# Performance work log

Measured on AMD Instinct MI355X. Metric: run time of the kernel, lower is better.

The kernel has to match this reference:

```python
import jax, jax.numpy as jnp
import numpy as np

B, W, IN, H, Z, D = 32, 256, 4096, 1024, 100, 100


def setup_inputs() -> dict:
    key = jax.random.key(0)
    ks = jax.random.split(key, 10)
    s = lambda k, shape, sc=0.02: jax.random.normal(k, shape, dtype=jnp.float32) * sc
    return {
        "x": jax.random.normal(ks[0], (B, W, IN), jnp.float32),
        # GRU params (torch layout: gates ordered r, z, n)
        "W_ih": s(ks[1], (3 * H, IN)),
        "W_hh": s(ks[2], (3 * H, H)),
        "b_ih": jnp.zeros((3 * H,), jnp.float32),
        "b_hh": jnp.zeros((3 * H,), jnp.float32),
        # dense / mu / sigma heads
        "Wd": s(ks[3], (D, Z + H)),
        "bd": jnp.zeros((D,), jnp.float32),
        "Wmu": s(ks[4], (Z, D)),
        "bmu": jnp.zeros((Z,), jnp.float32),
        "Wsig": s(ks[5], (Z, D)),
        "bsig": jnp.zeros((Z,), jnp.float32),
        # planar normalizing flow
        "u": jax.random.normal(ks[6], (1,), jnp.float32),
        "Wpnf": s(ks[7], (Z, Z)),
        "bpnf": jnp.zeros((Z,), jnp.float32),
        # torch.rand_like -> uniform [0,1), one draw per timestep: [W, B, Z]
        "noise": jax.random.uniform(ks[8], (W, B, Z), jnp.float32),
    }


def reference(x, W_ih, W_hh, b_ih, b_hh, Wd, bd, Wmu, bmu, Wsig, bsig, u, Wpnf, bpnf, noise):
    Bv = x.shape[0]
    Hd = W_hh.shape[1]
    Zd = Wmu.shape[0]
    # hoist input projection out of the recurrence: [W, B, 3H]
    xW = jnp.einsum('bwf,gf->wbg', x, W_ih) + b_ih

    def step(carry, inp):
        h, z_t = carry
        gi, eps = inp
        gh = h @ W_hh.T + b_hh
        gi_r, gi_z, gi_n = jnp.split(gi, 3, axis=-1)
        gh_r, gh_z, gh_n = jnp.split(gh, 3, axis=-1)
        r = jax.nn.sigmoid(gi_r + gh_r)
        zg = jax.nn.sigmoid(gi_z + gh_z)
        n = jnp.tanh(gi_n + r * gh_n)
        h_new = (1.0 - zg) * n + zg * h
        dense_out = jnp.concatenate([z_t, h_new], axis=-1) @ Wd.T + bd
        mu_t = dense_out @ Wmu.T + bmu
        lv_t = jax.nn.softplus(dense_out @ Wsig.T + bsig)  # module calls this "logvar"
        z_new = mu_t + jnp.exp(0.5 * lv_t) * eps  # reparam with uniform noise (as in source)
        z_new = z_new + u * jnp.tanh(z_new @ Wpnf.T + bpnf)  # planar flow
        return (h_new, z_new), (z_new, mu_t, lv_t)

    h0 = jnp.zeros((Bv, Hd), x.dtype)
    z0 = jnp.zeros((Bv, Zd), x.dtype)
    _, (z, mu, lv) = jax.lax.scan(step, (h0, z0), (xW, noise))
    # [W,B,Z] -> [B,W,Z]
    return (jnp.swapaxes(z, 0, 1), jnp.swapaxes(mu, 0, 1), jnp.swapaxes(lv, 0, 1))
```

## Files before the change

### kernel.cpp

```cpp
#include <hip/hip_runtime.h>
#include <stdint.h>


#define MFMA16 __builtin_amdgcn_mfma_f32_16x16x32_bf16

using f32x4  = __attribute__((ext_vector_type(4))) float;
using bf16x8 = __attribute__((ext_vector_type(8))) short;

static constexpr int NB_MM  = 64;
static constexpr int NB_ALL = 65;
static constexpr int TPB    = 1024;
static constexpr int WSTEPS = 256;

static constexpr int HS_STRIDE = 1032;
static constexpr int SM_HS    = 66048;
static constexpr int SM_TOTAL = 123648;

__device__ __align__(256) unsigned short g_gi[8192u * 3072u];
__device__ __align__(256) unsigned short g_hb[2 * 32 * 1024];
__device__ __align__(256) unsigned       g_bar[64];
__device__ unsigned g_flag;

__device__ __forceinline__ float bf2f(unsigned short v){
  unsigned u = ((unsigned)v) << 16;
  return __builtin_bit_cast(float, u);
}
__device__ __forceinline__ unsigned short f2bf(float f){
  unsigned u = __builtin_bit_cast(unsigned, f);
  u += 0x7FFFu + ((u >> 16) & 1u);
  return (unsigned short)(u >> 16);
}
__device__ __forceinline__ float ldin(const void* p, size_t i){
  return g_flag ? ((const float*)p)[i] : bf2f(((const unsigned short*)p)[i]);
}
__device__ __forceinline__ unsigned short ldbf(const void* p, size_t i){
  return g_flag ? f2bf(((const float*)p)[i]) : ((const unsigned short*)p)[i];
}
__device__ __forceinline__ void stout(void* p, size_t i, float v){
  if (g_flag) ((float*)p)[i] = v;
  else        ((unsigned short*)p)[i] = f2bf(v);
}
__device__ __forceinline__ void ld16(const void* p, size_t idx,
                                     uint4* lo, uint4* hi){
  if (g_flag){
    const float* f = (const float*)p + idx;
    float4 a = *(const float4*)(f);
    float4 b = *(const float4*)(f + 4);
    float4 c = *(const float4*)(f + 8);
    float4 d = *(const float4*)(f + 12);
    unsigned short s[16];
    s[0]=f2bf(a.x); s[1]=f2bf(a.y); s[2]=f2bf(a.z); s[3]=f2bf(a.w);
    s[4]=f2bf(b.x); s[5]=f2bf(b.y); s[6]=f2bf(b.z); s[7]=f2bf(b.w);
    s[8]=f2bf(c.x); s[9]=f2bf(c.y); s[10]=f2bf(c.z); s[11]=f2bf(c.w);
    s[12]=f2bf(d.x); s[13]=f2bf(d.y); s[14]=f2bf(d.z); s[15]=f2bf(d.w);
    *lo = *(uint4*)s; *hi = *(uint4*)(s + 8);
  } else {
    const unsigned short* q = (const unsigned short*)p + idx;
    *lo = *(const uint4*)q; *hi = *(const uint4*)(q + 8);
  }
}
__device__ __forceinline__ float sigm(float x){ return 1.f / (1.f + __expf(-x)); }
__device__ __forceinline__ float sane(float x, float lim){
  return fminf(fmaxf(x, -lim), lim);
}

__global__ void k_probe(const void* noise){
  if (threadIdx.x == 0 && blockIdx.x == 0){
    const unsigned* w = (const unsigned*)noise;
    unsigned f = 0;
    for (int k = 0; k < 16; ++k)
      if ((w[k] & 0xFFFFu) > 0x3F80u) f = 1u;
    g_flag = f;
  }
}

__global__ void k_state_init(){
  int i = blockIdx.x * blockDim.x + threadIdx.x;
  if (i < 32768) ((unsigned*)g_hb)[i] = 0u;
  else if (i < 32832) g_bar[i - 32768] = 0u;
}

__global__ __launch_bounds__(256) void k_gemm_gi(
    const void* __restrict__ x,
    const void* __restrict__ Wih,
    const void* __restrict__ bih)
{
  __shared__ unsigned short As[128 * 40];
  __shared__ unsigned short Bs[128 * 40];
  const int tm = blockIdx.x & 63;
  const int tn = blockIdx.x >> 6;
  const int m0 = tm * 128, n0 = tn * 128;
  const int t  = threadIdx.x;
  const int wave = t >> 6, lane = t & 63;
  const int wm = wave & 1, wn = wave >> 1;
  const int ln = lane & 15, kg = lane >> 4;

  const int srow = t >> 1;
  const int skc  = (t & 1) * 16;
  const int m  = m0 + srow;
  const int bb = m & 31, ww = m >> 5;
  const size_t aoff = ((size_t)(bb * 256 + ww)) * 4096 + skc;
  const size_t boff = ((size_t)(n0 + srow)) * 4096 + skc;
  unsigned short* asl = &As[srow * 40 + skc];
  unsigned short* bsl = &Bs[srow * 40 + skc];

  f32x4 acc[4][4];
#pragma unroll
  for (int i = 0; i < 4; ++i)
#pragma unroll
    for (int j = 0; j < 4; ++j) acc[i][j] = (f32x4){0.f, 0.f, 0.f, 0.f};

  uint4 av, av2, bv, bv2;
  ld16(x,   aoff, &av, &av2);
  ld16(Wih, boff, &bv, &bv2);

  for (int k0 = 0; k0 < 4096; k0 += 32){
    __syncthreads();
    *(uint4*)asl = av;  *(uint4*)(asl + 8) = av2;
    *(uint4*)bsl = bv;  *(uint4*)(bsl + 8) = bv2;
    __syncthreads();
    if (k0 + 32 < 4096){
      ld16(x,   aoff + k0 + 32, &av, &av2);
      ld16(Wih, boff + k0 + 32, &bv, &bv2);
    }
    bf16x8 af[4], bfv[4];
#pragma unroll
    for (int mt = 0; mt < 4; ++mt)
      af[mt] = *(const bf16x8*)&As[(wm * 64 + mt * 16 + ln) * 40 + kg * 8];
#pragma unroll
    for (int nt = 0; nt < 4; ++nt)
      bfv[nt] = *(const bf16x8*)&Bs[(wn * 64 + nt * 16 + ln) * 40 + kg * 8];
#pragma unroll
    for (int mt = 0; mt < 4; ++mt)
#pragma unroll
      for (int nt = 0; nt < 4; ++nt)
        acc[mt][nt] = MFMA16(af[mt], bfv[nt], acc[mt][nt], 0, 0, 0);
  }

#pragma unroll
  for (int nt = 0; nt < 4; ++nt){
    const int gc = n0 + wn * 64 + nt * 16 + ln;
    const float bias = ldin(bih, gc);
#pragma unroll
    for (int mt = 0; mt < 4; ++mt){
      const int rb = m0 + wm * 64 + mt * 16 + kg * 4;
#pragma unroll
      for (int r = 0; r < 4; ++r)
        g_gi[(size_t)(rb + r) * 3072 + gc] = f2bf(acc[mt][nt][r] + bias);
    }
  }
}

struct P2Args {
  const void* Whh;
  const void* bhh;
  const void* Wd;
  const void* bd;
  const void* Wmu;
  const void* bmu;
  const void* Wsig;
  const void* bsig;
  const void* u;
  const void* Wpnf;
  const void* bpnf;
  const void* noise;
  void*       out;
};

__device__ __forceinline__ void gridbar(){
  __syncthreads();
  if (threadIdx.x == 0){
    unsigned arr = __hip_atomic_fetch_add(&g_bar[0], 1u, __ATOMIC_RELAXED,
                                          __HIP_MEMORY_SCOPE_AGENT);
    unsigned target = arr - (arr % NB_ALL) + NB_ALL;
    while (__hip_atomic_load(&g_bar[0], __ATOMIC_RELAXED,
                             __HIP_MEMORY_SCOPE_AGENT) < target)
      __builtin_amdgcn_s_sleep(2);
  }
  __syncthreads();
  __builtin_amdgcn_sched_barrier(0);
}

__device__ __forceinline__ void stage_h(unsigned short* hs, int slot, int tid){
  const unsigned long long* src =
      (const unsigned long long*)(g_hb + (size_t)slot * 32768);
#pragma unroll
  for (int k = 0; k < 8; ++k){
    const int idx = tid + k * TPB;
    unsigned long long v = __hip_atomic_load(src + idx, __ATOMIC_RELAXED,
                                             __HIP_MEMORY_SCOPE_AGENT);
    const int row = idx >> 8;
    const int col = (idx & 255) * 4;
    *(unsigned long long*)&hs[row * HS_STRIDE + col] = v;
  }
}

__global__ __launch_bounds__(TPB) void k_recur(P2Args a)
{
  __shared__ __align__(16) char smem[SM_TOTAL];
  const int tid  = threadIdx.x;
  const int wv   = tid >> 6;
  const int lane = tid & 63;
  const int ln   = lane & 15, kg = lane >> 4;
  unsigned short* hs = (unsigned short*)smem;

  if (blockIdx.x < NB_MM){
    float*          gh   = (float*)(smem + SM_HS);
    unsigned short* hout = (unsigned short*)(smem + SM_HS + 12288);
    const int c0  = blockIdx.x * 16;
    const bool act = (wv < 12);
    const int mt = wv & 1, nt = (wv >> 1) % 3, kh = wv / 6;

    bf16x8 bfrag[16];
    if (act){
      const size_t base = (size_t)(nt * 1024 + c0 + ln) * 1024 + kh * 512 + kg * 8;
      for (int ks = 0; ks < 16; ++ks){
        unsigned short tmp[8];
#pragma unroll
        for (int q = 0; q < 8; ++q) tmp[q] = ldbf(a.Whh, base + ks * 32 + q);
        bfrag[ks] = *(bf16x8*)tmp;
      }
    }

    float bhr = 0.f, bhz = 0.f, bhn = 0.f;
    const int eb = tid >> 4, ej = tid & 15;
    if (tid < 512){
      bhr = ldin(a.bhh, c0 + ej);
      bhz = ldin(a.bhh, 1024 + c0 + ej);
      bhn = ldin(a.bhh, 2048 + c0 + ej);
    }
    float h_old = 0.f;

    for (int i = 0; i <= WSTEPS; ++i){
      if (i < WSTEPS){
        float gir = 0.f, giz = 0.f, gin = 0.f;
        if (tid < 512){
          const size_t go = ((size_t)i * 32 + eb) * 3072 + c0 + ej;
          gir = sane(bf2f(g_gi[go]),        1e4f);
          giz = sane(bf2f(g_gi[go + 1024]), 1e4f);
          gin = sane(bf2f(g_gi[go + 2048]), 1e4f);
        }
        stage_h(hs, i & 1, tid);
        __syncthreads();
        if (act){
          f32x4 acc = (f32x4){0.f, 0.f, 0.f, 0.f};
          const unsigned short* ap = &hs[(mt * 16 + ln) * HS_STRIDE + kh * 512 + kg * 8];
#pragma unroll
          for (int ks = 0; ks < 16; ++ks){
            bf16x8 af = *(const bf16x8*)(ap + ks * 32);
            acc = MFMA16(af, bfrag[ks], acc, 0, 0, 0);
          }
          float* g = gh + (size_t)kh * 1536;
#pragma unroll
          for (int r = 0; r < 4; ++r)
            g[(mt * 16 + kg * 4 + r) * 48 + nt * 16 + ln] = acc[r];
        }
        __syncthreads();
        if (tid < 512){
          const float ghr = gh[eb*48 + ej]      + gh[1536 + eb*48 + ej]      + bhr;
          const float ghz = gh[eb*48 + 16 + ej] + gh[1536 + eb*48 + 16 + ej] + bhz;
          const float ghn = gh[eb*48 + 32 + ej] + gh[1536 + eb*48 + 32 + ej] + bhn;
          const float r  = sigm(gir + ghr);
          const float zg = sigm(giz + ghz);
          const float n  = tanhf(gin + r * ghn);
          const float hn = (1.f - zg) * n + zg * h_old;
          h_old = hn;
          hout[eb * 16 + ej] = f2bf(hn);
        }
        __syncthreads();
        if (tid < 128){
          const int r = tid >> 2, q = tid & 3;
          unsigned long long v = *(const unsigned long long*)&hout[r * 16 + q * 4];
          unsigned long long* dst = (unsigned long long*)
              (g_hb + (size_t)((i + 1) & 1) * 32768 + (size_t)r * 1024 + c0) + q;
          __hip_atomic_store(dst, v, __ATOMIC_RELAXED, __HIP_MEMORY_SCOPE_AGENT);
        }
      }
      gridbar();
    }
  } else {
    unsigned short* zbf = (unsigned short*)(smem + SM_HS);
    unsigned short* abf = (unsigned short*)(smem + SM_HS + 8704);
    char*  scr   = smem + SM_HS + 17408;
    float* dacc0 = (float*)scr;
    float* dacc1 = (float*)(scr + 14336);
    float* msout = (float*)scr;
    float* zpre  = (float*)(scr + 25600);
    float* pnfo  = (float*)scr;
    float* ldsb  = (float*)(smem + SM_HS + 55808);

    for (int idx = tid; idx < 32 * 136; idx += TPB){ zbf[idx] = 0; abf[idx] = 0; }
    if (tid < 400){
      float v;
      if      (tid < 100) v = ldin(a.bd,   tid);
      else if (tid < 200) v = ldin(a.bmu,  tid - 100);
      else if (tid < 300) v = ldin(a.bsig, tid - 200);
      else                v = ldin(a.bpnf, tid - 300);
      ldsb[tid] = v;
    }
    const float uval = ldin(a.u, 0);

    const int nt_h = wv >> 1, khh = wv & 1;
    bf16x8 fH[16], fZ[2], fMS[4], fP[4];
    if (wv < 14){
      const int d = nt_h * 16 + ln;
      for (int ks = 0; ks < 16; ++ks){
        bf16x8 v;
        for (int q = 0; q < 8; ++q){
          const int k = khh * 512 + ks * 32 + kg * 8 + q;
          v[q] = (d < 100) ? (short)ldbf(a.Wd, (size_t)d * 1124 + 100 + k) : (short)0;
        }
        fH[ks] = v;
      }
      for (int q2 = 0; q2 < 2; ++q2){
        bf16x8 v;
        for (int q = 0; q < 8; ++q){
          const int c = (khh * 2 + q2) * 32 + kg * 8 + q;
          v[q] = (d < 100 && c < 100) ? (short)ldbf(a.Wd, (size_t)d * 1124 + c) : (short)0;
        }
        fZ[q2] = v;
      }
      for (int ks = 0; ks < 4; ++ks){
        bf16x8 v;
        for (int q = 0; q < 8; ++q){
          const int k = ks * 32 + kg * 8 + q;
          v[q] = (d < 100 && k < 100) ? (short)ldbf(a.Wpnf, (size_t)d * 100 + k) : (short)0;
        }
        fP[ks] = v;
      }
    }
    if (wv < 13){
      const int s = wv * 16 + ln;
      for (int ks = 0; ks < 4; ++ks){
        bf16x8 v;
        for (int q = 0; q < 8; ++q){
          const int k = ks * 32 + kg * 8 + q;
          short val = 0;
          if (k < 100){
            if (s < 100)      val = (short)ldbf(a.Wmu,  (size_t)s * 100 + k);
            else if (s < 200) val = (short)ldbf(a.Wsig, (size_t)(s - 100) * 100 + k);
          }
          v[q] = val;
        }
        fMS[ks] = v;
      }
    }

    for (int i = 0; i <= WSTEPS; ++i){
      if (i >= 1){
        const int t = i - 1;
        for (int idx = tid; idx < 2 * 32 * 112; idx += TPB) dacc0[idx] = 0.f;
        stage_h(hs, i & 1, tid);
        __syncthreads();
        if (wv < 14){
          f32x4 ac0 = (f32x4){0.f,0.f,0.f,0.f}, ac1 = (f32x4){0.f,0.f,0.f,0.f};
          const unsigned short* ap0 = &hs[ln * HS_STRIDE + khh * 512 + kg * 8];
          const unsigned short* ap1 = &hs[(16 + ln) * HS_STRIDE + khh * 512 + kg * 8];
#pragma unroll
          for (int ks = 0; ks < 16; ++ks){
            bf16x8 a0 = *(const bf16x8*)(ap0 + ks * 32);
            bf16x8 a1 = *(const bf16x8*)(ap1 + ks * 32);
            ac0 = MFMA16(a0, fH[ks], ac0, 0, 0, 0);
            ac1 = MFMA16(a1, fH[ks], ac1, 0, 0, 0);
          }
#pragma unroll
          for (int q2 = 0; q2 < 2; ++q2){
            const int kz = (khh * 2 + q2) * 32;
            bf16x8 z0 = *(const bf16x8*)&zbf[ln * 136 + kz + kg * 8];
            bf16x8 z1 = *(const bf16x8*)&zbf[(16 + ln) * 136 + kz + kg * 8];
            ac0 = MFMA16(z0, fZ[q2], ac0, 0, 0, 0);
            ac1 = MFMA16(z1, fZ[q2], ac1, 0, 0, 0);
          }
          float* dst = khh ? dacc1 : dacc0;
#pragma unroll
          for (int r = 0; r < 4; ++r){
            dst[(kg * 4 + r) * 112 + nt_h * 16 + ln]      = ac0[r];
            dst[(16 + kg * 4 + r) * 112 + nt_h * 16 + ln] = ac1[r];
          }
        }
        __syncthreads();
        if (tid < 800){
#pragma unroll
          for (int q = 0; q < 4; ++q){
            const int e = tid + 800 * q, b = e / 100, d = e - b * 100;
            const float v = sane(dacc0[b * 112 + d] + dacc1[b * 112 + d] + ldsb[d], 1e4f);
            abf[b * 136 + d] = f2bf(v);
          }
        }
        __syncthreads();
        if (wv < 13){
          f32x4 m0 = (f32x4){0.f,0.f,0.f,0.f}, m1 = (f32x4){0.f,0.f,0.f,0.f};
#pragma unroll
          for (int ks = 0; ks < 4; ++ks){
            bf16x8 a0 = *(const bf16x8*)&abf[ln * 136 + ks * 32 + kg * 8];
            bf16x8 a1 = *(const bf16x8*)&abf[(16 + ln) * 136 + ks * 32 + kg * 8];
            m0 = MFMA16(a0, fMS[ks], m0, 0, 0, 0);
            m1 = MFMA16(a1, fMS[ks], m1, 0, 0, 0);
          }
          const int s = wv * 16 + ln;
          if (s < 200){
#pragma unroll
            for (int r = 0; r < 4; ++r){
              msout[(kg * 4 + r) * 200 + s]      = m0[r];
              msout[(16 + kg * 4 + r) * 200 + s] = m1[r];
            }
          }
        }
        __syncthreads();
        if (tid < 800){
#pragma unroll
          for (int q = 0; q < 4; ++q){
            const int e = tid + 800 * q, b = e / 100, d = e - b * 100;
            const float mu = sane(msout[b * 200 + d] + ldsb[100 + d], 1e4f);
            float sg = msout[b * 200 + 100 + d] + ldsb[200 + d];
            sg = fminf(fmaxf(sg, -1e4f), 80.f);
            const float lv = fmaxf(sg, 0.f) + log1pf(__expf(-fabsf(sg)));
            const float eps = ldin(a.noise, ((size_t)t * 32 + b) * 100 + d);
            const float zp = sane(mu + __expf(0.5f * lv) * eps, 1e4f);
            const size_t ob = ((size_t)b * 256 + t) * 100 + d;
            stout(a.out, 819200 + ob, mu);
            stout(a.out, 1638400 + ob, lv);
            zpre[b * 100 + d] = zp;
            abf[b * 136 + d] = f2bf(zp);
          }
        }
        __syncthreads();
        if (wv < 14){
          const int pm = wv & 1, pn = wv >> 1;
          f32x4 pc = (f32x4){0.f,0.f,0.f,0.f};
#pragma unroll
          for (int ks = 0; ks < 4; ++ks){
            bf16x8 av = *(const bf16x8*)&abf[(pm * 16 + ln) * 136 + ks * 32 + kg * 8];
            pc = MFMA16(av, fP[ks], pc, 0, 0, 0);
          }
#pragma unroll
          for (int r = 0; r < 4; ++r)
            pnfo[(pm * 16 + kg * 4 + r) * 112 + pn * 16 + ln] = pc[r];
        }
        __syncthreads();
        if (tid < 800){
#pragma unroll
          for (int q = 0; q < 4; ++q){
            const int e = tid + 800 * q, b = e / 100, d = e - b * 100;
            const float zp = zpre[b * 100 + d];
            const float pv = sane(pnfo[b * 112 + d] + ldsb[300 + d], 1e4f);
            const float zf = sane(zp + uval * tanhf(pv), 1e4f);
            stout(a.out, ((size_t)b * 256 + t) * 100 + d, zf);
            zbf[b * 136 + d] = f2bf(zf);
          }
        }
      }
      gridbar();
    }
  }
}

extern "C" void kernel_launch(void* const* d_in, const int* in_sizes, int n_in,
                              void* d_out, int out_size, void* d_ws, size_t ws_size,
                              hipStream_t stream)
{
  const void* x     = d_in[0];
  const void* Wih   = d_in[1];
  const void* Whh   = d_in[2];
  const void* bih   = d_in[3];
  const void* bhh   = d_in[4];
  const void* Wd    = d_in[5];
  const void* bd    = d_in[6];
  const void* Wmu   = d_in[7];
  const void* bmu   = d_in[8];
  const void* Wsig  = d_in[9];
  const void* bsig  = d_in[10];
  const void* u     = d_in[11];
  const void* Wpnf  = d_in[12];
  const void* bpnf  = d_in[13];
  const void* noise = d_in[14];
  (void)d_ws; (void)ws_size;

  k_probe<<<dim3(1), dim3(64), 0, stream>>>(noise);
  k_state_init<<<dim3(129), dim3(256), 0, stream>>>();
  k_gemm_gi<<<dim3(1536), dim3(256), 0, stream>>>(x, Wih, bih);

  P2Args args{Whh, bhh, Wd, bd, Wmu, bmu, Wsig, bsig, u, Wpnf, bpnf, noise, d_out};
  k_recur<<<dim3(NB_ALL), dim3(TPB), 0, stream>>>(args);
}
```

Measured before the change: 5.306 ms.

## Distribute grid barrier counters and XOR-swizzle LDS hidden-state layout

The grid barrier now spreads arrivals over 8 counters on separate cache lines, each block incrementing one chosen by block index. Eight lanes poll all counters and sum them with shuffles against a monotonically increasing target, instead of all 65 blocks contending on one atomic. The hidden-state LDS tile also drops the padded row stride for a 2048-byte stride with an XOR swizzle, which avoids bank conflicts and frees some shared memory. The barrier runs 257 times per launch, so per-barrier latency matters, but polling eight counters adds memory traffic on each spin.

```diff
diff --git a/kernel.cpp b/kernel.cpp
--- a/kernel.cpp
+++ b/kernel.cpp
@@ -12,13 +12,12 @@
 static constexpr int TPB    = 1024;
 static constexpr int WSTEPS = 256;
 
-static constexpr int HS_STRIDE = 1032;
-static constexpr int SM_HS    = 66048;
-static constexpr int SM_TOTAL = 123648;
+static constexpr int SM_HS    = 65536;
+static constexpr int SM_TOTAL = 122944;
 
 __device__ __align__(256) unsigned short g_gi[8192u * 3072u];
 __device__ __align__(256) unsigned short g_hb[2 * 32 * 1024];
-__device__ __align__(256) unsigned       g_bar[64];
+__device__ __align__(256) unsigned       g_bar[256];
 __device__ unsigned g_flag;
 
 __device__ __forceinline__ float bf2f(unsigned short v){
@@ -77,7 +76,7 @@
 __global__ void k_state_init(){
   int i = blockIdx.x * blockDim.x + threadIdx.x;
   if (i < 32768) ((unsigned*)g_hb)[i] = 0u;
-  else if (i < 32832) g_bar[i - 32768] = 0u;
+  else if (i < 33024) g_bar[i - 32768] = 0u;
 }
 
 __global__ __launch_bounds__(256) void k_gemm_gi(
@@ -167,21 +166,31 @@
   void*       out;
 };
 
-__device__ __forceinline__ void gridbar(){
+__device__ __forceinline__ void gridbar(unsigned target){
   __syncthreads();
-  if (threadIdx.x == 0){
-    unsigned arr = __hip_atomic_fetch_add(&g_bar[0], 1u, __ATOMIC_RELAXED,
-                                          __HIP_MEMORY_SCOPE_AGENT);
-    unsigned target = arr - (arr % NB_ALL) + NB_ALL;
-    while (__hip_atomic_load(&g_bar[0], __ATOMIC_RELAXED,
-                             __HIP_MEMORY_SCOPE_AGENT) < target)
-      __builtin_amdgcn_s_sleep(2);
+  if (threadIdx.x < 8){
+    if (threadIdx.x == 0)
+      __hip_atomic_fetch_add(&g_bar[(blockIdx.x & 7) * 32], 1u,
+                             __ATOMIC_RELAXED, __HIP_MEMORY_SCOPE_AGENT);
+    for (;;){
+      unsigned s = __hip_atomic_load(&g_bar[threadIdx.x * 32],
+                                     __ATOMIC_RELAXED, __HIP_MEMORY_SCOPE_AGENT);
+      s += __shfl_xor(s, 1);
+      s += __shfl_xor(s, 2);
+      s += __shfl_xor(s, 4);
+      if (s >= target) break;
+      __builtin_amdgcn_s_sleep(1);
+    }
   }
   __syncthreads();
   __builtin_amdgcn_sched_barrier(0);
 }
 
-__device__ __forceinline__ void stage_h(unsigned short* hs, int slot, int tid){
+__device__ __forceinline__ char* lds_h(char* hsbase, int row, int off){
+  return hsbase + row * 2048 + (off ^ ((row & 7) << 4));
+}
+
+__device__ __forceinline__ void stage_h(char* hsbase, int slot, int tid){
   const unsigned long long* src =
       (const unsigned long long*)(g_hb + (size_t)slot * 32768);
 #pragma unroll
@@ -190,8 +199,8 @@
     unsigned long long v = __hip_atomic_load(src + idx, __ATOMIC_RELAXED,
                                              __HIP_MEMORY_SCOPE_AGENT);
     const int row = idx >> 8;
-    const int col = (idx & 255) * 4;
-    *(unsigned long long*)&hs[row * HS_STRIDE + col] = v;
+    const int off = (idx & 255) * 8;
+    *(unsigned long long*)lds_h(hsbase, row, off) = v;
   }
 }
 
@@ -202,7 +211,6 @@
   const int wv   = tid >> 6;
   const int lane = tid & 63;
   const int ln   = lane & 15, kg = lane >> 4;
-  unsigned short* hs = (unsigned short*)smem;
 
   if (blockIdx.x < NB_MM){
     float*          gh   = (float*)(smem + SM_HS);
@@ -240,14 +248,15 @@
           giz = sane(bf2f(g_gi[go + 1024]), 1e4f);
           gin = sane(bf2f(g_gi[go + 2048]), 1e4f);
         }
-        stage_h(hs, i & 1, tid);
+        stage_h(smem, i & 1, tid);
         __syncthreads();
         if (act){
           f32x4 acc = (f32x4){0.f, 0.f, 0.f, 0.f};
-          const unsigned short* ap = &hs[(mt * 16 + ln) * HS_STRIDE + kh * 512 + kg * 8];
+          const int row = mt * 16 + ln;
 #pragma unroll
           for (int ks = 0; ks < 16; ++ks){
-            bf16x8 af = *(const bf16x8*)(ap + ks * 32);
+            bf16x8 af = *(const bf16x8*)lds_h(smem, row,
+                              kh * 1024 + kg * 16 + ks * 64);
             acc = MFMA16(af, bfrag[ks], acc, 0, 0, 0);
           }
           float* g = gh + (size_t)kh * 1536;
@@ -276,7 +285,7 @@
           __hip_atomic_store(dst, v, __ATOMIC_RELAXED, __HIP_MEMORY_SCOPE_AGENT);
         }
       }
-      gridbar();
+      gridbar((unsigned)(i + 1) * NB_ALL);
     }
   } else {
     unsigned short* zbf = (unsigned short*)(smem + SM_HS);
@@ -350,16 +359,15 @@
       if (i >= 1){
         const int t = i - 1;
         for (int idx = tid; idx < 2 * 32 * 112; idx += TPB) dacc0[idx] = 0.f;
-        stage_h(hs, i & 1, tid);
+        stage_h(smem, i & 1, tid);
         __syncthreads();
         if (wv < 14){
           f32x4 ac0 = (f32x4){0.f,0.f,0.f,0.f}, ac1 = (f32x4){0.f,0.f,0.f,0.f};
-          const unsigned short* ap0 = &hs[ln * HS_STRIDE + khh * 512 + kg * 8];
-          const unsigned short* ap1 = &hs[(16 + ln) * HS_STRIDE + khh * 512 + kg * 8];
 #pragma unroll
           for (int ks = 0; ks < 16; ++ks){
-            bf16x8 a0 = *(const bf16x8*)(ap0 + ks * 32);
-            bf16x8 a1 = *(const bf16x8*)(ap1 + ks * 32);
+            const int off = khh * 1024 + kg * 16 + ks * 64;
+            bf16x8 a0 = *(const bf16x8*)lds_h(smem, ln,      off);
+            bf16x8 a1 = *(const bf16x8*)lds_h(smem, 16 + ln, off);
             ac0 = MFMA16(a0, fH[ks], ac0, 0, 0, 0);
             ac1 = MFMA16(a1, fH[ks], ac1, 0, 0, 0);
           }
@@ -450,7 +458,7 @@
           }
         }
       }
-      gridbar();
+      gridbar((unsigned)(i + 1) * NB_ALL);
     }
   }
 }
```

Result: slower. 5.583 ms (+5.2%).
